# Performance work log

Hardware: AMD Instinct MI355X
Metric: run time of the kernel (lower is better)

The kernel has to match this reference:

```python
import jax, jax.numpy as jnp
import numpy as np

B, S, D, H = 4, 2048, 1024, 16
HD = D // H


def setup_inputs() -> dict:
    key = jax.random.key(0)
    ks = jax.random.split(key, 12)
    sc = 1.0 / np.sqrt(D)
    inp = {
        'q': jax.random.normal(ks[0], (B, S, D), jnp.float32),
        'k': jax.random.normal(ks[1], (B, S, D), jnp.float32),
        'v': jax.random.normal(ks[2], (B, S, D), jnp.float32),
        # causal mask: 1 where masked (upper triangle), broadcasts over batch/heads
        'mask': jnp.triu(jnp.ones((S, S), jnp.float32), k=1),
        'Wq': jax.random.normal(ks[3], (D, D), jnp.float32) * sc,
        'bq': jax.random.normal(ks[4], (D,), jnp.float32) * sc,
        'Wk': jax.random.normal(ks[5], (D, D), jnp.float32) * sc,
        'bk': jax.random.normal(ks[6], (D,), jnp.float32) * sc,
        'Wv': jax.random.normal(ks[7], (D, D), jnp.float32) * sc,
        'bv': jax.random.normal(ks[8], (D,), jnp.float32) * sc,
        'Wo': jax.random.normal(ks[9], (D, D), jnp.float32) * sc,
        'bo': jax.random.normal(ks[10], (D,), jnp.float32) * sc,
    }
    return inp


def _split_heads(x):
    # [B,S,D] -> [B,H,S,HD]
    return x.reshape(B, S, H, HD).transpose(0, 2, 1, 3)


def reference(q, k, v, mask, Wq, bq, Wk, bk, Wv, bv, Wo, bo):
    qw = q @ Wq + bq
    kw = k @ Wk + bk
    vw = v @ Wv + bv
    qh, kh, vh = _split_heads(qw), _split_heads(kw), _split_heads(vw)
    scores = jnp.einsum('bhqd,bhkd->bhqk', qh, kh) / jnp.sqrt(jnp.float32(HD))
    scores = scores + mask * (-1e20)
    weights = jax.nn.softmax(scores, axis=-1)
    attn = jnp.einsum('bhqk,bhkd->bhqd', weights, vh)
    attn = attn.transpose(0, 2, 1, 3).reshape(B, S, D)
    return attn @ Wo + bo
```

## Files before the change

kernel.cpp:

```cpp
#include <hip/hip_runtime.h>
#include <hip/hip_bf16.h>
#include <stdint.h>

#define B_ 4
#define S_ 2048
#define D_ 1024
#define H_ 16
#define HD_ 64

typedef __bf16 bf16_t;
typedef __bf16 bf16x8 __attribute__((ext_vector_type(8)));
typedef __bf16 bf16x2_t __attribute__((ext_vector_type(2)));
typedef float f32x4 __attribute__((ext_vector_type(4)));
typedef int i32x4 __attribute__((ext_vector_type(4)));

#define MFMA(a, b, c) __builtin_amdgcn_mfma_f32_16x16x32_bf16((a), (b), (c), 0, 0, 0)
#define LOG2E 1.44269504088896340736f

__device__ __forceinline__ void gload_lds16(const void* g, void* l) {
  __builtin_amdgcn_global_load_lds(
      (const __attribute__((address_space(1))) uint32_t*)g,
      (__attribute__((address_space(3))) uint32_t*)l, 16, 0, 0);
}

__global__ __launch_bounds__(256) void wt_kernel(const float* __restrict__ Wq,
                                                 const float* __restrict__ Wk,
                                                 const float* __restrict__ Wv,
                                                 const float* __restrict__ Wo,
                                                 bf16_t* __restrict__ wt0) {
  __shared__ float t[32][33];
  const int z = blockIdx.z;
  const float* w_ = z == 0 ? Wq : (z == 1 ? Wk : (z == 2 ? Wv : Wo));
  bf16_t* wt = wt0 + (size_t)z * (1u << 20);
  const int tx = threadIdx.x & 31, ty = threadIdx.x >> 5;
  const int n0 = blockIdx.x * 32, k0 = blockIdx.y * 32;
#pragma unroll
  for (int i = 0; i < 4; i++)
    t[ty + i * 8][tx] = w_[(size_t)(k0 + ty + i * 8) * D_ + n0 + tx];
  __syncthreads();
#pragma unroll
  for (int i = 0; i < 4; i++)
    wt[(size_t)(n0 + ty + i * 8) * D_ + k0 + tx] = (bf16_t)t[tx][ty + i * 8];
}

__global__ __launch_bounds__(256) void conv_kernel(const float* __restrict__ q,
                                                   const float* __restrict__ k,
                                                   const float* __restrict__ v,
                                                   bf16_t* __restrict__ out) {
  const int z = blockIdx.z;
  const float* src = z == 0 ? q : (z == 1 ? k : v);
  bf16_t* dst = out + (size_t)z * 8388608u;
  const size_t i = ((size_t)blockIdx.x * 256 + threadIdx.x) * 8;
  float4 x0 = *(const float4*)(src + i);
  float4 x1 = *(const float4*)(src + i + 4);
  bf16x8 vv;
  vv[0] = (bf16_t)x0.x; vv[1] = (bf16_t)x0.y; vv[2] = (bf16_t)x0.z; vv[3] = (bf16_t)x0.w;
  vv[4] = (bf16_t)x1.x; vv[5] = (bf16_t)x1.y; vv[6] = (bf16_t)x1.z; vv[7] = (bf16_t)x1.w;
  *(bf16x8*)(dst + i) = vv;
}

template <bool QKV>
__global__ __launch_bounds__(256) void mm_kernel(const bf16_t* __restrict__ A0,
                                                 const bf16_t* __restrict__ wt0,
                                                 const float* __restrict__ b0,
                                                 const float* __restrict__ b1,
                                                 const float* __restrict__ b2,
                                                 void* __restrict__ out0) {
  __shared__ bf16_t smem[32768];

  const int z = QKV ? blockIdx.z : 0;
  const bf16_t* A = A0 + (size_t)z * 8388608u;
  const bf16_t* WT = wt0 + (size_t)z * 1048576u;
  const float* bias = QKV ? (z == 0 ? b0 : (z == 1 ? b1 : b2)) : b0;

  const int tid = threadIdx.x;
  const int w = tid >> 6, l = tid & 63;
  const int lr = l & 15, lg = l >> 4;
  const int wm = w >> 1, wn = w & 1;
  const int ib = (int)blockIdx.y * 8 + (int)blockIdx.x;
  const int swz = (ib & 7) * 64 + (ib >> 3);
  const int m0 = (swz >> 3) * 128, n0 = (swz & 7) * 128;

  const int row0 = tid >> 3;
  const int ks = (tid & 7) ^ (row0 & 7);
  const bf16_t* aS = A + (size_t)(m0 + row0) * 1024 + ks * 8;
  const bf16_t* bS = WT + (size_t)(n0 + row0) * 1024 + ks * 8;
  const int wsl = w * 512;

  f32x4 acc[4][4];
#pragma unroll
  for (int mt = 0; mt < 4; mt++)
#pragma unroll
    for (int nt = 0; nt < 4; nt++) {
      f32x4 zz = {0.f, 0.f, 0.f, 0.f};
      acc[mt][nt] = zz;
    }

#define STAGE(bi, kt)                                                   \
  do {                                                                  \
    bf16_t* ad = smem + (bi) * 16384 + wsl;                             \
    bf16_t* bd = smem + (bi) * 16384 + 8192 + wsl;                      \
    _Pragma("unroll") for (int c = 0; c < 4; c++) {                     \
      gload_lds16(bS + (size_t)c * 32768 + (kt), bd + c * 2048);        \
      gload_lds16(aS + (size_t)c * 32768 + (kt), ad + c * 2048);        \
    }                                                                   \
  } while (0)

  STAGE(0, 0);
  STAGE(1, 64);
  asm volatile("s_waitcnt vmcnt(8)" ::: "memory");
  __builtin_amdgcn_s_barrier();
  __builtin_amdgcn_sched_barrier(0);

  int buf = 0;
  for (int jt = 0; jt < 16; ++jt) {
    const bf16_t* alds = smem + buf * 16384;
    const bf16_t* blds = alds + 8192;
#pragma unroll
    for (int kk = 0; kk < 2; kk++) {
      bf16x8 af[4], bfr[4];
#pragma unroll
      for (int mt = 0; mt < 4; mt++) {
        int row = wm * 64 + mt * 16 + lr;
        int kc = kk * 4 + lg;
        af[mt] = *reinterpret_cast<const bf16x8*>(alds + row * 64 + ((kc ^ (row & 7)) * 8));
      }
#pragma unroll
      for (int nt = 0; nt < 4; nt++) {
        int row = wn * 64 + nt * 16 + lr;
        int kc = kk * 4 + lg;
        bfr[nt] = *reinterpret_cast<const bf16x8*>(blds + row * 64 + ((kc ^ (row & 7)) * 8));
      }
#pragma unroll
      for (int mt = 0; mt < 4; mt++)
#pragma unroll
        for (int nt = 0; nt < 4; nt++)
          acc[mt][nt] = MFMA(af[mt], bfr[nt], acc[mt][nt]);
    }
    if (jt == 15) break;
    __builtin_amdgcn_sched_barrier(0);
    __builtin_amdgcn_s_barrier();
    __builtin_amdgcn_sched_barrier(0);
    const int tn = (jt + 2 < 16) ? jt + 2 : 15;
    STAGE(buf, tn * 64);
    asm volatile("s_waitcnt vmcnt(8)" ::: "memory");
    __builtin_amdgcn_s_barrier();
    __builtin_amdgcn_sched_barrier(0);
    buf ^= 1;
  }
#undef STAGE

  float bn[4];
#pragma unroll
  for (int nt = 0; nt < 4; nt++) bn[nt] = bias[n0 + wn * 64 + nt * 16 + lr];

  if (!QKV) {
    float* out = (float*)out0;
#pragma unroll
    for (int mt = 0; mt < 4; mt++)
#pragma unroll
      for (int nt = 0; nt < 4; nt++)
#pragma unroll
        for (int r = 0; r < 4; r++) {
          int m = m0 + wm * 64 + mt * 16 + lg * 4 + r;
          int n = n0 + wn * 64 + nt * 16 + lr;
          out[(size_t)m * D_ + n] = acc[mt][nt][r] + bn[nt];
        }
  } else if (z != 2) {
    bf16_t* out = (bf16_t*)out0 + (size_t)z * 8388608u;
    const float sc = z == 0 ? 0.125f * LOG2E : 1.0f;
#pragma unroll
    for (int mt = 0; mt < 4; mt++)
#pragma unroll
      for (int nt = 0; nt < 4; nt++)
#pragma unroll
        for (int r = 0; r < 4; r++) {
          int m = m0 + wm * 64 + mt * 16 + lg * 4 + r;
          int n = n0 + wn * 64 + nt * 16 + lr;
          float v = (acc[mt][nt][r] + bn[nt]) * sc;
          int b = m >> 11, s = m & 2047, h = n >> 6, hd = n & 63;
          out[(((size_t)(b * H_ + h) * S_ + s) << 6) + hd] = (bf16_t)v;
        }
  } else {
    bf16_t* out = (bf16_t*)out0 + (size_t)z * 8388608u;
    __syncthreads();
#pragma unroll
    for (int mt = 0; mt < 4; mt++)
#pragma unroll
      for (int nt = 0; nt < 4; nt++)
#pragma unroll
        for (int r = 0; r < 4; r++) {
          int ml = wm * 64 + mt * 16 + lg * 4 + r;
          int nl = wn * 64 + nt * 16 + lr;
          smem[nl * 136 + ml] = (bf16_t)(acc[mt][nt][r] + bn[nt]);
        }
    __syncthreads();
    const int b = m0 >> 11, sbase = m0 & 2047;
#pragma unroll
    for (int c = 0; c < 8; c++) {
      int ci = c * 256 + tid;
      int dl = ci >> 4, sc2 = ci & 15;
      int n = n0 + dl, h = n >> 6, hd = n & 63;
      bf16x8 v = *reinterpret_cast<const bf16x8*>(smem + dl * 136 + sc2 * 8);
      *reinterpret_cast<bf16x8*>(out + ((size_t)((b * H_ + h) << 6) + hd) * S_ + sbase + sc2 * 8) = v;
    }
  }
}

__global__ __launch_bounds__(256) void attn_k(const bf16_t* __restrict__ qh,
                                              const bf16_t* __restrict__ kh,
                                              const bf16_t* __restrict__ vt,
                                              bf16_t* __restrict__ attn) {
  __shared__ bf16_t kbuf[2][4096];
  __shared__ bf16_t vbuf[2][4096];

  const int tid = threadIdx.x, w = tid >> 6, l = tid & 63;
  const int lr = l & 15, lg = l >> 4;

  const int ib = (int)blockIdx.y * 16 + (int)blockIdx.x;
  const int xcd = ib & 7;
  const int bh = xcd * 8 + ((ib >> 3) & 7);
  const int jq = ib >> 6, gq = jq >> 2, rq = jq & 3;
  const int qt = gq == 0 ? 15 - rq : (gq == 1 ? rq : (gq == 2 ? 11 - rq : 4 + rq));
  const int b = bh >> 4, h = bh & 15;

  const int zr0 = tid >> 3, kc = tid & 7;
  const int sks = kc ^ (zr0 & 7);
  const int kprow0 = ((zr0 >> 5) & 1) * 32 + ((zr0 >> 2) & 3) * 8 + ((zr0 >> 4) & 1) * 4 + (zr0 & 3);
  const int zr1 = 32 + zr0;
  const int kprow1 = ((zr1 >> 5) & 1) * 32 + ((zr1 >> 2) & 3) * 8 + ((zr1 >> 4) & 1) * 4 + (zr1 & 3);
  const bf16_t* kbase0 = kh + ((size_t)bh * S_ + kprow0) * HD_ + sks * 8;
  const bf16_t* kbase1 = kh + ((size_t)bh * S_ + kprow1) * HD_ + sks * 8;
  const bf16_t* vbase0 = vt + ((size_t)bh * HD_ + zr0) * S_ + sks * 8;
  const bf16_t* vbase1 = vt + ((size_t)bh * HD_ + zr1) * S_ + sks * 8;

  const int xs7 = lr & 7;
  const int koffA = lr * 64 + ((lg ^ xs7) << 3);
  const int koffB = lr * 64 + (((lg ^ xs7) ^ 4) << 3);
  const int rowlim0 = w * 32 + lr;
  const int rowlim1 = w * 32 + 16 + lr;
  const int wact = w * 32 + 31;
  const int wsl = w * 512;

  bf16x8 ones;
#pragma unroll
  for (int i = 0; i < 8; i++) ones[i] = (bf16_t)1.0f;

  const int q0 = qt * 128 + w * 32;
  const int jend = 2 * qt + 1;

  const bf16_t* qp0 = qh + ((size_t)bh * S_ + q0 + lr) * HD_ + lg * 8;
  const bf16_t* qp1 = qp0 + 16 * HD_;
  bf16x8 qf00 = *(const bf16x8*)qp0;
  bf16x8 qf01 = *(const bf16x8*)(qp0 + 32);
  bf16x8 qf10 = *(const bf16x8*)qp1;
  bf16x8 qf11 = *(const bf16x8*)(qp1 + 32);

  f32x4 o0[4], o1[4], os0, os1;
#pragma unroll
  for (int nt = 0; nt < 4; nt++) {
    f32x4 z = {0.f, 0.f, 0.f, 0.f};
    o0[nt] = z; o1[nt] = z;
  }
  {
    f32x4 z = {0.f, 0.f, 0.f, 0.f};
    os0 = z; os1 = z;
  }

  const bf16_t *ks0 = kbase0, *ks1 = kbase1, *vs0 = vbase0, *vs1 = vbase1;
  int jsrc = 0;

#define ISSUE_STAGE(kd, vd)                                     \
  do {                                                          \
    gload_lds16(ks0, (kd));                                     \
    gload_lds16(ks1, (kd) + 2048);                              \
    gload_lds16(vs0, (vd));                                     \
    gload_lds16(vs1, (vd) + 2048);                              \
    if (jsrc < jend) {                                          \
      ks0 += 64 * HD_; ks1 += 64 * HD_; vs0 += 64; vs1 += 64;   \
      jsrc++;                                                   \
    }                                                           \
  } while (0)

  const bf16_t *rK = kbuf[0], *rV = vbuf[0];
  const bf16_t *rKn = kbuf[1], *rVn = vbuf[1];
  bf16_t *wK = &kbuf[1][wsl], *wV = &vbuf[1][wsl];
  bf16_t *wKn = &kbuf[0][wsl], *wVn = &vbuf[0][wsl];

  ISSUE_STAGE(wKn, wVn);

  for (int jt = 0; jt <= jend; jt++) {
    ISSUE_STAGE(wK, wV);
    asm volatile("s_waitcnt vmcnt(4)" ::: "memory");
    __builtin_amdgcn_s_barrier();
    __builtin_amdgcn_sched_barrier(0);

    const int doff = jt * 64 - qt * 128;
    if (doff <= wact) {
      f32x4 s0[4], s1[4];
      __builtin_amdgcn_s_setprio(1);
#pragma unroll
      for (int nt = 0; nt < 4; nt++) {
        bf16x8 kf0 = *(const bf16x8*)(rK + koffA + nt * 1024);
        bf16x8 kf1 = *(const bf16x8*)(rK + koffB + nt * 1024);
        f32x4 a = {0.f, 0.f, 0.f, 0.f};
        a = MFMA(kf0, qf00, a);
        a = MFMA(kf1, qf01, a);
        s0[nt] = a;
        f32x4 a2 = {0.f, 0.f, 0.f, 0.f};
        a2 = MFMA(kf0, qf10, a2);
        a2 = MFMA(kf1, qf11, a2);
        s1[nt] = a2;
      }
      __builtin_amdgcn_s_setprio(0);
      if (doff >= 0) {
#pragma unroll
        for (int nt = 0; nt < 4; nt++) {
          int kvb = doff + ((nt >> 1) << 5) + ((nt & 1) << 2) + lg * 8;
#pragma unroll
          for (int r = 0; r < 4; r++) {
            if (kvb + r > rowlim0) s0[nt][r] = -1e30f;
            if (kvb + r > rowlim1) s1[nt][r] = -1e30f;
          }
        }
      }
#pragma unroll
      for (int nt = 0; nt < 4; nt++)
#pragma unroll
        for (int r = 0; r < 4; r++) {
          s0[nt][r] = __builtin_amdgcn_exp2f(s0[nt][r]);
          s1[nt][r] = __builtin_amdgcn_exp2f(s1[nt][r]);
        }
      uint32_t pk0[8], pk1[8];
#pragma unroll
      for (int nt = 0; nt < 4; nt++) {
        bf16x2_t p0lo = {(bf16_t)s0[nt][0], (bf16_t)s0[nt][1]};
        bf16x2_t p0hi = {(bf16_t)s0[nt][2], (bf16_t)s0[nt][3]};
        pk0[nt * 2] = __builtin_bit_cast(uint32_t, p0lo);
        pk0[nt * 2 + 1] = __builtin_bit_cast(uint32_t, p0hi);
        bf16x2_t p1lo = {(bf16_t)s1[nt][0], (bf16_t)s1[nt][1]};
        bf16x2_t p1hi = {(bf16_t)s1[nt][2], (bf16_t)s1[nt][3]};
        pk1[nt * 2] = __builtin_bit_cast(uint32_t, p1lo);
        pk1[nt * 2 + 1] = __builtin_bit_cast(uint32_t, p1hi);
      }
      i32x4 w00 = {(int)pk0[0], (int)pk0[1], (int)pk0[2], (int)pk0[3]};
      i32x4 w01 = {(int)pk0[4], (int)pk0[5], (int)pk0[6], (int)pk0[7]};
      i32x4 w10 = {(int)pk1[0], (int)pk1[1], (int)pk1[2], (int)pk1[3]};
      i32x4 w11 = {(int)pk1[4], (int)pk1[5], (int)pk1[6], (int)pk1[7]};
      bf16x8 pa00 = __builtin_bit_cast(bf16x8, w00);
      bf16x8 pa01 = __builtin_bit_cast(bf16x8, w01);
      bf16x8 pa10 = __builtin_bit_cast(bf16x8, w10);
      bf16x8 pa11 = __builtin_bit_cast(bf16x8, w11);
      __builtin_amdgcn_s_setprio(1);
#pragma unroll
      for (int ntd = 0; ntd < 4; ntd++) {
        bf16x8 vf0 = *(const bf16x8*)(rV + koffA + ntd * 1024);
        bf16x8 vf1 = *(const bf16x8*)(rV + koffB + ntd * 1024);
        o0[ntd] = MFMA(pa00, vf0, o0[ntd]);
        o0[ntd] = MFMA(pa01, vf1, o0[ntd]);
        o1[ntd] = MFMA(pa10, vf0, o1[ntd]);
        o1[ntd] = MFMA(pa11, vf1, o1[ntd]);
      }
      os0 = MFMA(pa00, ones, os0);
      os0 = MFMA(pa01, ones, os0);
      os1 = MFMA(pa10, ones, os1);
      os1 = MFMA(pa11, ones, os1);
      __builtin_amdgcn_s_setprio(0);
    }

    __builtin_amdgcn_sched_barrier(0);
    __builtin_amdgcn_s_barrier();
    __builtin_amdgcn_sched_barrier(0);
    { const bf16_t* t = rK; rK = rKn; rKn = t; t = rV; rV = rVn; rVn = t; }
    { bf16_t* t = wK; wK = wKn; wKn = t; t = wV; wV = wVn; wVn = t; }
  }
#undef ISSUE_STAGE
#pragma unroll
  for (int r = 0; r < 4; r++) {
    float rinv0 = 1.f / os0[r];
    float rinv1 = 1.f / os1[r];
    int srw0 = q0 + lg * 4 + r;
    int srw1 = srw0 + 16;
#pragma unroll
    for (int ntd = 0; ntd < 4; ntd++) {
      attn[((size_t)(b * S_ + srw0)) * D_ + h * 64 + ntd * 16 + lr] =
          (bf16_t)(o0[ntd][r] * rinv0);
      attn[((size_t)(b * S_ + srw1)) * D_ + h * 64 + ntd * 16 + lr] =
          (bf16_t)(o1[ntd][r] * rinv1);
    }
  }
}

extern "C" void kernel_launch(void* const* d_in, const int* in_sizes, int n_in,
                              void* d_out, int out_size, void* d_ws, size_t ws_size,
                              hipStream_t stream) {
  (void)in_sizes; (void)n_in; (void)out_size; (void)ws_size;
  const float* q  = (const float*)d_in[0];
  const float* k  = (const float*)d_in[1];
  const float* v  = (const float*)d_in[2];
  const float* Wq = (const float*)d_in[4];
  const float* bq = (const float*)d_in[5];
  const float* Wk = (const float*)d_in[6];
  const float* bk = (const float*)d_in[7];
  const float* Wv = (const float*)d_in[8];
  const float* bv = (const float*)d_in[9];
  const float* Wo = (const float*)d_in[10];
  const float* bo = (const float*)d_in[11];

  char* ws = (char*)d_ws;
  bf16_t* wt0  = (bf16_t*)(ws + (0ull << 20));
  bf16_t* wto  = (bf16_t*)(ws + (6ull << 20));
  bf16_t* qkvb = (bf16_t*)(ws + (8ull << 20));
  bf16_t* qhb  = (bf16_t*)(ws + (56ull << 20));
  bf16_t* khb  = (bf16_t*)(ws + (72ull << 20));
  bf16_t* vtb  = (bf16_t*)(ws + (88ull << 20));
  bf16_t* atb  = (bf16_t*)(ws + (8ull << 20));

  dim3 tb(256);
  wt_kernel<<<dim3(32, 32, 4), tb, 0, stream>>>(Wq, Wk, Wv, Wo, wt0);
  conv_kernel<<<dim3(4096, 1, 3), tb, 0, stream>>>(q, k, v, qkvb);
  mm_kernel<true><<<dim3(8, 64, 3), tb, 0, stream>>>(qkvb, wt0, bq, bk, bv, qhb);
  attn_k<<<dim3(16, 64), tb, 0, stream>>>(qhb, khb, vtb, atb);
  mm_kernel<false><<<dim3(8, 64), tb, 0, stream>>>(atb, wto, bo, nullptr, nullptr, d_out);
}
```

Before: 157.1 us.

## Enlarge attention query tile to 256 rows per block, 64 per wave

Each attention block now handles 256 query rows instead of 128, with each wave processing four 16-row groups instead of two, so every K/V tile loaded into LDS is reused across twice as many queries. The grid halves to 512 blocks and the query-tile ordering for load balancing is simplified to a two-group scheme. This cuts K/V global and LDS traffic per unit of work but raises register pressure (more accumulators and Q fragments), lowers block count and may reduce occupancy. It also makes causal-load imbalance coarser.

```diff
diff --git a/kernel.cpp b/kernel.cpp
--- a/kernel.cpp
+++ b/kernel.cpp
@@ -217,11 +217,11 @@
   const int tid = threadIdx.x, w = tid >> 6, l = tid & 63;
   const int lr = l & 15, lg = l >> 4;
 
-  const int ib = (int)blockIdx.y * 16 + (int)blockIdx.x;
+  const int ib = (int)blockIdx.y * 8 + (int)blockIdx.x;
   const int xcd = ib & 7;
   const int bh = xcd * 8 + ((ib >> 3) & 7);
-  const int jq = ib >> 6, gq = jq >> 2, rq = jq & 3;
-  const int qt = gq == 0 ? 15 - rq : (gq == 1 ? rq : (gq == 2 ? 11 - rq : 4 + rq));
+  const int jq = ib >> 6;
+  const int qt = jq < 4 ? (7 - jq) : (jq - 4);
   const int b = bh >> 4, h = bh & 15;
 
   const int zr0 = tid >> 3, kc = tid & 7;
@@ -237,34 +237,31 @@
   const int xs7 = lr & 7;
   const int koffA = lr * 64 + ((lg ^ xs7) << 3);
   const int koffB = lr * 64 + (((lg ^ xs7) ^ 4) << 3);
-  const int rowlim0 = w * 32 + lr;
-  const int rowlim1 = w * 32 + 16 + lr;
-  const int wact = w * 32 + 31;
+  const int wact = w * 64 + 63;
   const int wsl = w * 512;
 
   bf16x8 ones;
 #pragma unroll
   for (int i = 0; i < 8; i++) ones[i] = (bf16_t)1.0f;
 
-  const int q0 = qt * 128 + w * 32;
-  const int jend = 2 * qt + 1;
-
-  const bf16_t* qp0 = qh + ((size_t)bh * S_ + q0 + lr) * HD_ + lg * 8;
-  const bf16_t* qp1 = qp0 + 16 * HD_;
-  bf16x8 qf00 = *(const bf16x8*)qp0;
-  bf16x8 qf01 = *(const bf16x8*)(qp0 + 32);
-  bf16x8 qf10 = *(const bf16x8*)qp1;
-  bf16x8 qf11 = *(const bf16x8*)(qp1 + 32);
-
-  f32x4 o0[4], o1[4], os0, os1;
-#pragma unroll
-  for (int nt = 0; nt < 4; nt++) {
+  const int q0 = qt * 256 + w * 64;
+  const int jend = 4 * qt + 3;
+
+  bf16x8 qf[4][2];
+#pragma unroll
+  for (int g = 0; g < 4; g++) {
+    const bf16_t* qp = qh + ((size_t)bh * S_ + q0 + g * 16 + lr) * HD_ + lg * 8;
+    qf[g][0] = *(const bf16x8*)qp;
+    qf[g][1] = *(const bf16x8*)(qp + 32);
+  }
+
+  f32x4 o[4][4], os[4];
+#pragma unroll
+  for (int g = 0; g < 4; g++) {
     f32x4 z = {0.f, 0.f, 0.f, 0.f};
-    o0[nt] = z; o1[nt] = z;
-  }
-  {
-    f32x4 z = {0.f, 0.f, 0.f, 0.f};
-    os0 = z; os1 = z;
+    os[g] = z;
+#pragma unroll
+    for (int nt = 0; nt < 4; nt++) o[g][nt] = z;
   }
 
   const bf16_t *ks0 = kbase0, *ks1 = kbase1, *vs0 = vbase0, *vs1 = vbase1;
@@ -295,22 +292,21 @@
     __builtin_amdgcn_s_barrier();
     __builtin_amdgcn_sched_barrier(0);
 
-    const int doff = jt * 64 - qt * 128;
+    const int doff = jt * 64 - qt * 256;
     if (doff <= wact) {
-      f32x4 s0[4], s1[4];
+      f32x4 s[4][4];
       __builtin_amdgcn_s_setprio(1);
 #pragma unroll
       for (int nt = 0; nt < 4; nt++) {
         bf16x8 kf0 = *(const bf16x8*)(rK + koffA + nt * 1024);
         bf16x8 kf1 = *(const bf16x8*)(rK + koffB + nt * 1024);
-        f32x4 a = {0.f, 0.f, 0.f, 0.f};
-        a = MFMA(kf0, qf00, a);
-        a = MFMA(kf1, qf01, a);
-        s0[nt] = a;
-        f32x4 a2 = {0.f, 0.f, 0.f, 0.f};
-        a2 = MFMA(kf0, qf10, a2);
-        a2 = MFMA(kf1, qf11, a2);
-        s1[nt] = a2;
+#pragma unroll
+        for (int g = 0; g < 4; g++) {
+          f32x4 a = {0.f, 0.f, 0.f, 0.f};
+          a = MFMA(kf0, qf[g][0], a);
+          a = MFMA(kf1, qf[g][1], a);
+          s[g][nt] = a;
+        }
       }
       __builtin_amdgcn_s_setprio(0);
       if (doff >= 0) {
@@ -318,53 +314,53 @@
         for (int nt = 0; nt < 4; nt++) {
           int kvb = doff + ((nt >> 1) << 5) + ((nt & 1) << 2) + lg * 8;
 #pragma unroll
-          for (int r = 0; r < 4; r++) {
-            if (kvb + r > rowlim0) s0[nt][r] = -1e30f;
-            if (kvb + r > rowlim1) s1[nt][r] = -1e30f;
+          for (int g = 0; g < 4; g++) {
+            int rowlim = w * 64 + g * 16 + lr;
+#pragma unroll
+            for (int r = 0; r < 4; r++)
+              if (kvb + r > rowlim) s[g][nt][r] = -1e30f;
           }
         }
       }
 #pragma unroll
-      for (int nt = 0; nt < 4; nt++)
-#pragma unroll
-        for (int r = 0; r < 4; r++) {
-          s0[nt][r] = __builtin_amdgcn_exp2f(s0[nt][r]);
-          s1[nt][r] = __builtin_amdgcn_exp2f(s1[nt][r]);
-        }
-      uint32_t pk0[8], pk1[8];
-#pragma unroll
-      for (int nt = 0; nt < 4; nt++) {
-        bf16x2_t p0lo = {(bf16_t)s0[nt][0], (bf16_t)s0[nt][1]};
-        bf16x2_t p0hi = {(bf16_t)s0[nt][2], (bf16_t)s0[nt][3]};
-        pk0[nt * 2] = __builtin_bit_cast(uint32_t, p0lo);
-        pk0[nt * 2 + 1] = __builtin_bit_cast(uint32_t, p0hi);
-        bf16x2_t p1lo = {(bf16_t)s1[nt][0], (bf16_t)s1[nt][1]};
-        bf16x2_t p1hi = {(bf16_t)s1[nt][2], (bf16_t)s1[nt][3]};
-        pk1[nt * 2] = __builtin_bit_cast(uint32_t, p1lo);
-        pk1[nt * 2 + 1] = __builtin_bit_cast(uint32_t, p1hi);
-      }
-      i32x4 w00 = {(int)pk0[0], (int)pk0[1], (int)pk0[2], (int)pk0[3]};
-      i32x4 w01 = {(int)pk0[4], (int)pk0[5], (int)pk0[6], (int)pk0[7]};
-      i32x4 w10 = {(int)pk1[0], (int)pk1[1], (int)pk1[2], (int)pk1[3]};
-      i32x4 w11 = {(int)pk1[4], (int)pk1[5], (int)pk1[6], (int)pk1[7]};
-      bf16x8 pa00 = __builtin_bit_cast(bf16x8, w00);
-      bf16x8 pa01 = __builtin_bit_cast(bf16x8, w01);
-      bf16x8 pa10 = __builtin_bit_cast(bf16x8, w10);
-      bf16x8 pa11 = __builtin_bit_cast(bf16x8, w11);
+      for (int g = 0; g < 4; g++)
+#pragma unroll
+        for (int nt = 0; nt < 4; nt++)
+#pragma unroll
+          for (int r = 0; r < 4; r++)
+            s[g][nt][r] = __builtin_amdgcn_exp2f(s[g][nt][r]);
+      bf16x8 pa[4][2];
+#pragma unroll
+      for (int g = 0; g < 4; g++) {
+        uint32_t pk[8];
+#pragma unroll
+        for (int nt = 0; nt < 4; nt++) {
+          bf16x2_t plo = {(bf16_t)s[g][nt][0], (bf16_t)s[g][nt][1]};
+          bf16x2_t phi = {(bf16_t)s[g][nt][2], (bf16_t)s[g][nt][3]};
+          pk[nt * 2] = __builtin_bit_cast(uint32_t, plo);
+          pk[nt * 2 + 1] = __builtin_bit_cast(uint32_t, phi);
+        }
+        i32x4 w0 = {(int)pk[0], (int)pk[1], (int)pk[2], (int)pk[3]};
+        i32x4 w1 = {(int)pk[4], (int)pk[5], (int)pk[6], (int)pk[7]};
+        pa[g][0] = __builtin_bit_cast(bf16x8, w0);
+        pa[g][1] = __builtin_bit_cast(bf16x8, w1);
+      }
       __builtin_amdgcn_s_setprio(1);
 #pragma unroll
       for (int ntd = 0; ntd < 4; ntd++) {
         bf16x8 vf0 = *(const bf16x8*)(rV + koffA + ntd * 1024);
         bf16x8 vf1 = *(const bf16x8*)(rV + koffB + ntd * 1024);
-        o0[ntd] = MFMA(pa00, vf0, o0[ntd]);
-        o0[ntd] = MFMA(pa01, vf1, o0[ntd]);
-        o1[ntd] = MFMA(pa10, vf0, o1[ntd]);
-        o1[ntd] = MFMA(pa11, vf1, o1[ntd]);
-      }
-      os0 = MFMA(pa00, ones, os0);
-      os0 = MFMA(pa01, ones, os0);
-      os1 = MFMA(pa10, ones, os1);
-      os1 = MFMA(pa11, ones, os1);
+#pragma unroll
+        for (int g = 0; g < 4; g++) {
+          o[g][ntd] = MFMA(pa[g][0], vf0, o[g][ntd]);
+          o[g][ntd] = MFMA(pa[g][1], vf1, o[g][ntd]);
+        }
+      }
+#pragma unroll
+      for (int g = 0; g < 4; g++) {
+        os[g] = MFMA(pa[g][0], ones, os[g]);
+        os[g] = MFMA(pa[g][1], ones, os[g]);
+      }
       __builtin_amdgcn_s_setprio(0);
     }
 
@@ -376,17 +372,15 @@
   }
 #undef ISSUE_STAGE
 #pragma unroll
-  for (int r = 0; r < 4; r++) {
-    float rinv0 = 1.f / os0[r];
-    float rinv1 = 1.f / os1[r];
-    int srw0 = q0 + lg * 4 + r;
-    int srw1 = srw0 + 16;
-#pragma unroll
-    for (int ntd = 0; ntd < 4; ntd++) {
-      attn[((size_t)(b * S_ + srw0)) * D_ + h * 64 + ntd * 16 + lr] =
-          (bf16_t)(o0[ntd][r] * rinv0);
-      attn[((size_t)(b * S_ + srw1)) * D_ + h * 64 + ntd * 16 + lr] =
-          (bf16_t)(o1[ntd][r] * rinv1);
+  for (int g = 0; g < 4; g++) {
+#pragma unroll
+    for (int r = 0; r < 4; r++) {
+      float rinv = 1.f / os[g][r];
+      int srw = q0 + g * 16 + lg * 4 + r;
+#pragma unroll
+      for (int ntd = 0; ntd < 4; ntd++)
+        attn[((size_t)(b * S_ + srw)) * D_ + h * 64 + ntd * 16 + lr] =
+            (bf16_t)(o[g][ntd][r] * rinv);
     }
   }
 }
@@ -420,6 +414,6 @@
   wt_kernel<<<dim3(32, 32, 4), tb, 0, stream>>>(Wq, Wk, Wv, Wo, wt0);
   conv_kernel<<<dim3(4096, 1, 3), tb, 0, stream>>>(q, k, v, qkvb);
   mm_kernel<true><<<dim3(8, 64, 3), tb, 0, stream>>>(qkvb, wt0, bq, bk, bv, qhb);
-  attn_k<<<dim3(16, 64), tb, 0, stream>>>(qhb, khb, vtb, atb);
+  attn_k<<<dim3(8, 64), tb, 0, stream>>>(qhb, khb, vtb, atb);
   mm_kernel<false><<<dim3(8, 64), tb, 0, stream>>>(atb, wto, bo, nullptr, nullptr, d_out);
 }
```

After: 189.4 us. +20.6%, slower.
